# Performance work log

Measured on AMD Instinct MI355X. Metric: run time of the kernel, lower is better.

Reference implementation:

```python
import jax, jax.numpy as jnp
import numpy as np
from functools import partial

B, S, T = 32, 64, 64
VS, VT = 32000, 32000
E, H = 256, 512            # embed_dim, encoder hidden per direction
DH = 2 * H                 # decoder hidden (= encoder_hidden_dim)
A = 128                    # attention_dim


def _p(key, shape, scale=0.05):
    return scale * jax.random.normal(key, shape, dtype=jnp.float32)


def setup_inputs() -> dict:
    key = jax.random.key(0)
    ks = jax.random.split(key, 32)
    inp = {
        'src': jax.random.randint(ks[0], (B, S), 0, VS),
        'tgt_input': jax.random.randint(ks[1], (B, T), 0, VT),
        # encoder
        'enc_emb': _p(ks[2], (VS, E)),
        'enc_Wih_f': _p(ks[3], (4 * H, E)), 'enc_Whh_f': _p(ks[4], (4 * H, H)),
        'enc_bih_f': _p(ks[5], (4 * H,)),  'enc_bhh_f': _p(ks[6], (4 * H,)),
        'enc_Wih_b': _p(ks[7], (4 * H, E)), 'enc_Whh_b': _p(ks[8], (4 * H, H)),
        'enc_bih_b': _p(ks[9], (4 * H,)),  'enc_bhh_b': _p(ks[10], (4 * H,)),
        # decoder
        'dec_emb': _p(ks[11], (VT, E)),
        'Wd': _p(ks[12], (A, DH)), 'bd': _p(ks[13], (A,)),
        'We': _p(ks[14], (A, DH)), 'be': _p(ks[15], (A,)),
        'v_att': _p(ks[16], (A,)), 'bv': _p(ks[17], ()),
        'dec_Wih': _p(ks[18], (4 * DH, E + DH)), 'dec_Whh': _p(ks[19], (4 * DH, DH)),
        'dec_bih': _p(ks[20], (4 * DH,)), 'dec_bhh': _p(ks[21], (4 * DH,)),
        'Wo': _p(ks[22], (VT, DH + DH)), 'bo': _p(ks[23], (VT,)),
    }
    return inp


def _lstm_cell(x, h, c, Wih, Whh, b):
    g = x @ Wih.T + h @ Whh.T + b
    i, f, gg, o = jnp.split(g, 4, axis=-1)  # PyTorch gate order: i,f,g,o
    i, f, o = jax.nn.sigmoid(i), jax.nn.sigmoid(f), jax.nn.sigmoid(o)
    c_new = f * c + i * jnp.tanh(gg)
    h_new = o * jnp.tanh(c_new)
    return h_new, c_new


def _lstm_scan(xs, Wih, Whh, b, reverse):
    # xs: [S,B,E] -> outputs [S,B,H] aligned with input positions, final (h,c)
    h0 = jnp.zeros((xs.shape[1], Whh.shape[1]), xs.dtype)
    def step(carry, x):
        h, c = carry
        h, c = _lstm_cell(x, h, c, Wih, Whh, b)
        return (h, c), h
    (hT, cT), hs = jax.lax.scan(step, (h0, h0), xs, reverse=reverse)
    return hs, hT, cT


def _forward(src, tgt_input, enc_emb,
             enc_Wih_f, enc_Whh_f, enc_bih_f, enc_bhh_f,
             enc_Wih_b, enc_Whh_b, enc_bih_b, enc_bhh_b,
             dec_emb, Wd, bd, We, be, v_att, bv,
             dec_Wih, dec_Whh, dec_bih, dec_bhh, Wo, bo):
    # ---- Encoder: bidirectional single-layer LSTM ----
    emb = enc_emb[src]                              # [B,S,E]
    xs = emb.transpose(1, 0, 2)                     # [S,B,E]
    hs_f, hT_f, cT_f = _lstm_scan(xs, enc_Wih_f, enc_Whh_f, enc_bih_f + enc_bhh_f, False)
    hs_b, hT_b, cT_b = _lstm_scan(xs, enc_Wih_b, enc_Whh_b, enc_bih_b + enc_bhh_b, True)
    enc_out = jnp.concatenate([hs_f, hs_b], axis=-1).transpose(1, 0, 2)  # [B,S,2H]
    h = jnp.concatenate([hT_f, hT_b], axis=-1)      # [B,DH]
    c = jnp.concatenate([cT_f, cT_b], axis=-1)

    # ---- Decoder with Bahdanau attention (full teacher forcing) ----
    enc_proj = enc_out @ We.T + be                  # [B,S,A] precomputed
    dec_b = dec_bih + dec_bhh
    tgt_emb = dec_emb[tgt_input].transpose(1, 0, 2)  # [T,B,E]

    def dec_step(carry, emb_t):
        h, c = carry
        dproj = h @ Wd.T + bd                       # [B,A]
        energy = jnp.tanh(dproj[:, None, :] + enc_proj)  # [B,S,A]
        scores = energy @ v_att + bv                # [B,S]
        w = jax.nn.softmax(scores, axis=1)
        ctx = jnp.einsum('bs,bsh->bh', w, enc_out)  # [B,DH]
        x = jnp.concatenate([emb_t, ctx], axis=-1)  # [B,E+DH]
        h_new, c_new = _lstm_cell(x, h, c, dec_Wih, dec_Whh, dec_b)
        logits = jnp.concatenate([h_new, ctx], axis=-1) @ Wo.T + bo  # [B,VT]
        return (h_new, c_new), logits

    _, logits = jax.lax.scan(dec_step, (h, c), tgt_emb)  # [T,B,VT]
    return logits.transpose(1, 0, 2)                     # [B,T,VT]


def reference(src, tgt_input, enc_emb,
              enc_Wih_f, enc_Whh_f, enc_bih_f, enc_bhh_f,
              enc_Wih_b, enc_Whh_b, enc_bih_b, enc_bhh_b,
              dec_emb, Wd, bd, We, be, v_att, bv,
              dec_Wih, dec_Whh, dec_bih, dec_bhh, Wo, bo):
    return _forward(src, tgt_input, enc_emb,
                    enc_Wih_f, enc_Whh_f, enc_bih_f, enc_bhh_f,
                    enc_Wih_b, enc_Whh_b, enc_bih_b, enc_bhh_b,
                    dec_emb, Wd, bd, We, be, v_att, bv,
                    dec_Wih, dec_Whh, dec_bih, dec_bhh, Wo, bo)
```

## Files before the change

### kernel.cpp

```cpp
#include <hip/hip_runtime.h>


using u16 = unsigned short;
using u32 = unsigned int;
using u64 = unsigned long long;
using f32x4 = __attribute__((ext_vector_type(4))) float;
using s16x8 = __attribute__((ext_vector_type(8))) short;
using u16x4 = __attribute__((ext_vector_type(4))) unsigned short;

__device__ __forceinline__ float sigm_(float x) { return 1.0f / (1.0f + expf(-x)); }
__device__ __forceinline__ float tanh_(float x) {
    float e = __expf(fminf(2.0f * x, 30.0f));
    return (e - 1.0f) / (e + 1.0f);
}

__device__ __forceinline__ u16 f2bf(float x) {
    u32 u = __float_as_uint(x);
    u += 0x7fffu + ((u >> 16) & 1u);
    return (u16)(u >> 16);
}
__device__ __forceinline__ u32 pk2(float a, float b) {
    return (u32)f2bf(a) | ((u32)f2bf(b) << 16);
}
__device__ __forceinline__ float bf2f(u16 v) {
    return __uint_as_float((u32)v << 16);
}

__device__ __forceinline__ void ast32(u32* p, u32 v) {
    __hip_atomic_store(p, v, __ATOMIC_RELAXED, __HIP_MEMORY_SCOPE_AGENT);
}

#define MFMA __builtin_amdgcn_mfma_f32_16x16x32_bf16

#define GLL(g, l) __builtin_amdgcn_global_load_lds( \
    (__attribute__((address_space(1))) void*)(g),   \
    (__attribute__((address_space(3))) void*)(l), 16, 0, 0)

__device__ __forceinline__ void gbar(int* cnt, int target) {
    asm volatile("s_waitcnt vmcnt(0) lgkmcnt(0)" ::: "memory");
    __syncthreads();
    if (threadIdx.x == 0) {
        __hip_atomic_fetch_add(cnt, 1, __ATOMIC_RELAXED, __HIP_MEMORY_SCOPE_AGENT);
        while (__hip_atomic_load(cnt, __ATOMIC_RELAXED, __HIP_MEMORY_SCOPE_AGENT) < target)
            __builtin_amdgcn_s_sleep(1);
    }
    __syncthreads();
}

__global__ __launch_bounds__(256) void k_zero(float* __restrict__ p, int n) {
    int i = blockIdx.x * 256 + threadIdx.x;
    if (i < n) p[i] = 0.0f;
}

__global__ __launch_bounds__(256) void k_cast_bf16(const float* __restrict__ in,
                                                   u16* __restrict__ outp, int n8) {
    int idx = blockIdx.x * 256 + threadIdx.x;
    if (idx >= n8) return;
    const f32x4* p = (const f32x4*)in + (size_t)idx * 2;
    f32x4 a = p[0], c = p[1];
    u32* o = (u32*)(outp + (size_t)idx * 8);
    o[0] = pk2(a.x, a.y); o[1] = pk2(a.z, a.w);
    o[2] = pk2(c.x, c.y); o[3] = pk2(c.z, c.w);
}

__global__ __launch_bounds__(256) void k_embed_bf(const int* __restrict__ tok,
                                                  const float* __restrict__ emb,
                                                  u16* __restrict__ outp) {
    int idx = blockIdx.x * 256 + threadIdx.x;
    int r = idx >> 6, e4 = idx & 63;
    int outer = r >> 5, b = r & 31;
    int tk = tok[b * 64 + outer];
    f32x4 v = ((const f32x4*)emb)[(size_t)tk * 64 + e4];
    u32* o = (u32*)(outp + (size_t)r * 256 + (e4 << 2));
    o[0] = pk2(v.x, v.y); o[1] = pk2(v.z, v.w);
}

__global__ __launch_bounds__(256) void k_prep_perm(
    const float* __restrict__ src, u16* __restrict__ dst,
    int J, int K4, int srcStride, int srcOff, int total)
{
    int idx = blockIdx.x * 256 + threadIdx.x;
    if (idx >= total) return;
    int n = idx / K4, kq = (idx - n * K4) << 2;
    int orig = (n & 3) * J + (n >> 2);
    f32x4 v = *(const f32x4*)(src + (size_t)orig * srcStride + srcOff + kq);
    u32* o = (u32*)(dst + (size_t)n * (K4 << 2) + kq);
    o[0] = pk2(v.x, v.y); o[1] = pk2(v.z, v.w);
}

__global__ __launch_bounds__(256) void k_prep_ws(
    const float* __restrict__ W, u16* __restrict__ dst)
{
    int idx = blockIdx.x * 256 + threadIdx.x;
    int n = idx >> 8, kp = idx & 255, k0 = kp << 1;
    int orig = (n & 3) * 512 + (n >> 2);
    const float* s = W + (size_t)orig * 512 + k0;
    int g = n >> 5, r = n & 31;
    int byteoff = (k0 << 1) ^ ((r & 7) << 4);
    *(u32*)((char*)dst + (size_t)g * 32768 + r * 1024 + byteoff) = pk2(s[0], s[1]);
}

__global__ __launch_bounds__(256) void k_prep_w2s(
    const float* __restrict__ Whh, const float* __restrict__ Wih, u16* __restrict__ dst)
{
    int idx = blockIdx.x * 256 + threadIdx.x;
    int n = idx >> 10, kp = idx & 1023, k0 = kp << 1;
    int orig = (n & 3) * 1024 + (n >> 2);
    const float* s = (k0 < 1024) ? (Whh + (size_t)orig * 1024 + k0)
                                 : (Wih + (size_t)orig * 1280 + 256 + (k0 - 1024));
    int g = n >> 5, r = n & 31;
    int byteoff = (k0 << 1) ^ ((r & 7) << 4);
    *(u32*)((char*)dst + (size_t)g * 131072 + r * 4096 + byteoff) = pk2(s[0], s[1]);
}

__global__ __launch_bounds__(256) void k_gemm_bf(
    const u16* __restrict__ A, const u16* __restrict__ B, int K,
    const float* __restrict__ b1, const float* __restrict__ b2, int biasJ,
    float* __restrict__ C, int ldc, int nM, int nN, int remapOut, int swz)
{
    __shared__ __align__(16) u16 As[128 * 32];
    __shared__ __align__(16) u16 Bs[128 * 32];
    int w = blockIdx.x;
    if (swz) { int cpx = (nM * nN) >> 3; w = (w & 7) * cpx + (w >> 3); }
    int bm = (w % nM) * 128, bn = (w / nM) * 128;
    int tid = threadIdx.x, wave = tid >> 6, lane = tid & 63;
    int wm = wave & 1, wn = wave >> 1;
    f32x4 acc[4][4] = {};

    int rA = wave * 32 + (lane >> 2);
    int cb2 = (lane & 3) * 16;
    const char* gA = (const char*)A + ((size_t)(bm + rA) * K) * 2 + cb2;
    const char* gB = (const char*)B + ((size_t)(bn + rA) * K) * 2 + cb2;
    size_t rowskip = (size_t)16 * K * 2;
    char* lA = (char*)As + wave * 2048;
    char* lB = (char*)Bs + wave * 2048;
    const u16* rdA = As + (wm * 64 + (lane & 15)) * 32 + (lane >> 4) * 8;
    const u16* rdB = Bs + (wn * 64 + (lane & 15)) * 32 + (lane >> 4) * 8;

    for (int k0 = 0; k0 < K; k0 += 32) {
        size_t kb = (size_t)k0 * 2;
        GLL(gA + kb, lA); GLL(gA + kb + rowskip, lA + 1024);
        GLL(gB + kb, lB); GLL(gB + kb + rowskip, lB + 1024);
        __syncthreads();
        s16x8 af[4], bfv[4];
#pragma unroll
        for (int m2 = 0; m2 < 4; ++m2) af[m2] = *(const s16x8*)(rdA + m2 * 512);
#pragma unroll
        for (int n2 = 0; n2 < 4; ++n2) bfv[n2] = *(const s16x8*)(rdB + n2 * 512);
#pragma unroll
        for (int m2 = 0; m2 < 4; ++m2)
#pragma unroll
            for (int n2 = 0; n2 < 4; ++n2)
                acc[m2][n2] = MFMA(af[m2], bfv[n2], acc[m2][n2], 0, 0, 0);
        __syncthreads();
    }

    int rbase = bm + wm * 64 + ((lane >> 4) << 2);
    int cbase = bn + wn * 64 + (lane & 15);
#pragma unroll
    for (int n2 = 0; n2 < 4; ++n2) {
        int col = cbase + n2 * 16;
        int bcol = biasJ ? ((col & 3) * biasJ + (col >> 2)) : col;
        float bias = (b1 ? b1[bcol] : 0.0f) + (b2 ? b2[bcol] : 0.0f);
#pragma unroll
        for (int m2 = 0; m2 < 4; ++m2) {
            f32x4 v = acc[m2][n2];
#pragma unroll
            for (int jj = 0; jj < 4; ++jj) {
                int row = rbase + m2 * 16 + jj;
                int orow = remapOut ? ((row & 31) * 64 + (row >> 5)) : row;
                C[(size_t)orow * ldc + col] = v[jj] + bias;
            }
        }
    }
}

__global__ __launch_bounds__(256, 1) void k_enc_persist(
    const u16* __restrict__ Wsf, const u16* __restrict__ Wsb,
    const float* __restrict__ Gfp, const float* __restrict__ Gbp,
    u16* __restrict__ henc,
    float* __restrict__ cfb,
    u16* __restrict__ encbf,
    int* __restrict__ bar)
{
    __shared__ __align__(16) char smem[50176];
    int tid = threadIdx.x, lane = tid & 63, q = tid >> 6;
    int dir = blockIdx.x >> 6, g = blockIdx.x & 63;
    const char* wsrc = (const char*)(dir ? Wsb : Wsf) + (size_t)g * 32768;
#pragma unroll
    for (int it = 0; it < 8; ++it)
        GLL(wsrc + it * 4096 + tid * 16, smem + it * 4096 + tid * 16);
    __syncthreads();

    float* sacc = (float*)(smem + 32768);
    u16* hst = (u16*)(smem + 49664);
    const float* Gp = dir ? Gbp : Gfp;
    float* cB = cfb + dir * 16384;
    int lr = lane & 15, lk = (lane >> 4) << 3;
    int bb = tid & 31, jl = tid >> 5;
    int n0 = g * 32, j = g * 8 + jl;
    int bi = 0;

    for (int s = 0; s < 64; ++s) {
        const u16* hA = henc + (size_t)s * 32768 + dir * 16384;
        s16x8 afr[8];
#pragma unroll
        for (int it = 0; it < 4; ++it) {
            int ke = q * 128 + it * 32 + lk;
            afr[2 * it]     = *(const s16x8*)(hA + lr * 512 + ke);
            afr[2 * it + 1] = *(const s16x8*)(hA + (lr + 16) * 512 + ke);
        }
        f32x4 acc00 = {}, acc01 = {}, acc10 = {}, acc11 = {};
#pragma unroll
        for (int it = 0; it < 4; ++it) {
            int ke = q * 128 + it * 32 + lk;
            int kb = ke << 1;
            s16x8 b0 = *(const s16x8*)(smem + lr * 1024 + (kb ^ ((lr & 7) << 4)));
            int r1 = lr + 16;
            s16x8 b1 = *(const s16x8*)(smem + r1 * 1024 + (kb ^ ((r1 & 7) << 4)));
            acc00 = MFMA(afr[2 * it], b0, acc00, 0, 0, 0);
            acc01 = MFMA(afr[2 * it], b1, acc01, 0, 0, 0);
            acc10 = MFMA(afr[2 * it + 1], b0, acc10, 0, 0, 0);
            acc11 = MFMA(afr[2 * it + 1], b1, acc11, 0, 0, 0);
        }
        int rw = (lane >> 4) << 2;
#pragma unroll
        for (int rr = 0; rr < 4; ++rr) {
            sacc[q * 1056 + (rw + rr) * 33 + lr]        = acc00[rr];
            sacc[q * 1056 + (rw + rr) * 33 + 16 + lr]   = acc01[rr];
            sacc[q * 1056 + (16 + rw + rr) * 33 + lr]      = acc10[rr];
            sacc[q * 1056 + (16 + rw + rr) * 33 + 16 + lr] = acc11[rr];
        }
        __syncthreads();
        {
            int t = dir ? (63 - s) : s;
            int c4 = jl << 2;
            float gi = 0, gf = 0, gg = 0, go2 = 0;
#pragma unroll
            for (int q2 = 0; q2 < 4; ++q2) {
                const float* sp = sacc + q2 * 1056 + bb * 33 + c4;
                gi += sp[0]; gf += sp[1]; gg += sp[2]; go2 += sp[3];
            }
            f32x4 p4 = *(const f32x4*)(Gp + ((size_t)(t * 32 + bb)) * 2048 + n0 + c4);
            gi += p4.x; gf += p4.y; gg += p4.z; go2 += p4.w;
            float* cp = cB + bb * 512 + j;
            float cn = sigm_(gf) * cp[0] + sigm_(gi) * tanhf(gg);
            cp[0] = cn;
            float h = sigm_(go2) * tanhf(cn);
            u16 h16 = f2bf(h);
            encbf[((size_t)(bb * 64 + t)) * 1024 + dir * 512 + j] = h16;
            hst[bb * 8 + jl] = h16;
        }
        __syncthreads();
        if (tid < 128) {
            int bb2 = tid >> 2, p2 = tid & 3;
            u32 wv = (u32)hst[bb2 * 8 + 2 * p2] | ((u32)hst[bb2 * 8 + 2 * p2 + 1] << 16);
            ast32((u32*)(henc + (size_t)(s + 1) * 32768 + dir * 16384) + bb2 * 256 + g * 4 + p2, wv);
        }
        gbar(bar, (++bi) * 128);
    }
}

__global__ __launch_bounds__(256) void k_dec_init(
    const u16* __restrict__ henc, const float* __restrict__ cfb,
    u16* __restrict__ hcarr, float* __restrict__ cd)
{
    int idx = blockIdx.x * 256 + threadIdx.x;
    int b = idx >> 10, j = idx & 1023;
    int dir = (j >> 9), jj = j & 511;
    hcarr[b * 2048 + j] = henc[(size_t)64 * 32768 + dir * 16384 + b * 512 + jj];
    cd[b * 1024 + j] = cfb[dir * 16384 + b * 512 + jj];
}

__global__ __launch_bounds__(256, 1) void k_dec_persist(
    const u16* __restrict__ W2s, const u16* __restrict__ encbf,
    const float* __restrict__ Prep,
    const u16* __restrict__ Wd_bf, const float* __restrict__ bd,
    const float* __restrict__ eproj, const float* __restrict__ v_att,
    const float* __restrict__ bv,
    u16* __restrict__ hcarr, float* __restrict__ cd, u16* __restrict__ Abf,
    int* __restrict__ bar)
{
    __shared__ __align__(16) char smem[148480];
    int blk = blockIdx.x, tid = threadIdx.x, lane = tid & 63, q = tid >> 6;
    bool isgate = blk < 128;
    {
        const char* src = isgate ? ((const char*)W2s + (size_t)blk * 131072)
                                 : ((const char*)encbf + (size_t)(blk - 128) * 131072);
#pragma unroll
        for (int it = 0; it < 32; ++it)
            GLL(src + it * 4096 + tid * 16, smem + it * 4096 + tid * 16);
    }
    __syncthreads();

    float* sacc = (float*)(smem + 131072);
    u16* hst    = (u16*)(smem + 147968);
    float* hsh  = (float*)(smem + 131072);
    float* red  = (float*)(smem + 135168);
    float* dp   = (float*)(smem + 136192);
    float* sc   = (float*)(smem + 136704);

    int lr = lane & 15, lk = (lane >> 4) << 3;
    int bb = tid & 31, jl = tid >> 5;
    int n0 = blk * 32, j = blk * 8 + jl;
    int b = blk - 128;
    int bi = 0;

    for (int t = 0; t < 64; ++t) {
        const u16* hcT = hcarr + (size_t)t * 65536;
        f32x4 acc00 = {}, acc01 = {}, acc10 = {}, acc11 = {};
        f32x4 p4;
        if (isgate) {
            p4 = *(const f32x4*)(Prep + ((size_t)(t * 32 + bb)) * 4096 + n0 + (jl << 2));
            s16x8 afr[16];
#pragma unroll
            for (int it = 0; it < 8; ++it) {
                int ke = q * 256 + it * 32 + lk;
                afr[2 * it]     = *(const s16x8*)(hcT + lr * 2048 + ke);
                afr[2 * it + 1] = *(const s16x8*)(hcT + (lr + 16) * 2048 + ke);
            }
#pragma unroll
            for (int it = 0; it < 8; ++it) {
                int ke = q * 256 + it * 32 + lk;
                int kb = ke << 1;
                s16x8 b0 = *(const s16x8*)(smem + lr * 4096 + (kb ^ ((lr & 7) << 4)));
                int r1 = lr + 16;
                s16x8 b1 = *(const s16x8*)(smem + r1 * 4096 + (kb ^ ((r1 & 7) << 4)));
                acc00 = MFMA(afr[2 * it], b0, acc00, 0, 0, 0);
                acc01 = MFMA(afr[2 * it], b1, acc01, 0, 0, 0);
                acc10 = MFMA(afr[2 * it + 1], b0, acc10, 0, 0, 0);
                acc11 = MFMA(afr[2 * it + 1], b1, acc11, 0, 0, 0);
            }
        } else {
            {
                u16x4 hv = *(const u16x4*)(hcT + b * 2048 + (tid << 2));
                hsh[(tid << 2) + 0] = bf2f(hv.x);
                hsh[(tid << 2) + 1] = bf2f(hv.y);
                hsh[(tid << 2) + 2] = bf2f(hv.z);
                hsh[(tid << 2) + 3] = bf2f(hv.w);
            }
            __syncthreads();
            {
                int a = tid & 127, half = tid >> 7;
                const u16* wr = Wd_bf + ((size_t)a << 10) + (half << 9);
                const float* hh = hsh + (half << 9);
                float s0 = 0, s1 = 0, s2 = 0, s3 = 0;
#pragma unroll 4
                for (int k = 0; k < 512; k += 32) {
                    s16x8 w0 = *(const s16x8*)(wr + k);
                    s16x8 w1 = *(const s16x8*)(wr + k + 8);
                    s16x8 w2 = *(const s16x8*)(wr + k + 16);
                    s16x8 w3 = *(const s16x8*)(wr + k + 24);
#pragma unroll
                    for (int e = 0; e < 8; ++e) {
                        s0 += bf2f((u16)w0[e]) * hh[k + e];
                        s1 += bf2f((u16)w1[e]) * hh[k + 8 + e];
                        s2 += bf2f((u16)w2[e]) * hh[k + 16 + e];
                        s3 += bf2f((u16)w3[e]) * hh[k + 24 + e];
                    }
                }
                red[tid] = (s0 + s1) + (s2 + s3);
            }
            __syncthreads();
            if (tid < 128) dp[tid] = red[tid] + red[tid + 128] + bd[tid];
            __syncthreads();
            {
                int si = tid >> 2, qq = tid & 3;
                const float* ep = eproj + ((size_t)(b * 64 + si)) * 128 + qq * 32;
                float s = 0.0f;
#pragma unroll 8
                for (int a2 = 0; a2 < 32; ++a2)
                    s += v_att[qq * 32 + a2] * tanh_(dp[qq * 32 + a2] + ep[a2]);
                red[tid] = s;
            }
            __syncthreads();
            if (tid < 64) {
                float x = red[tid * 4] + red[tid * 4 + 1] + red[tid * 4 + 2] + red[tid * 4 + 3] + bv[0];
                float mx = x;
#pragma unroll
                for (int off = 32; off; off >>= 1) mx = fmaxf(mx, __shfl_xor(mx, off));
                float e = __expf(x - mx), ss = e;
#pragma unroll
                for (int off = 32; off; off >>= 1) ss += __shfl_xor(ss, off);
                sc[tid] = e / ss;
            }
            __syncthreads();
            {
                const u16* eL = (const u16*)smem;
                int c0i = tid << 2;
                float c0 = 0, c1 = 0, c2 = 0, c3 = 0;
                for (int s2 = 0; s2 < 64; ++s2) {
                    float wgt = sc[s2];
                    u16x4 rp = *(const u16x4*)(eL + s2 * 1024 + c0i);
                    c0 += wgt * bf2f(rp.x); c1 += wgt * bf2f(rp.y);
                    c2 += wgt * bf2f(rp.z); c3 += wgt * bf2f(rp.w);
                }
                u32 w0 = pk2(c0, c1), w1 = pk2(c2, c3);
                u32* hw = (u32*)hcT + b * 1024 + 512 + (tid << 1);
                ast32(hw, w0); ast32(hw + 1, w1);
                u32* aw = (u32*)(Abf + ((size_t)(t * 32 + b)) * 2048 + 1024 + c0i);
                aw[0] = w0; aw[1] = w1;
            }
        }
        gbar(bar, (++bi) * 160);
        if (isgate) {
            s16x8 afr[16];
#pragma unroll
            for (int it = 0; it < 8; ++it) {
                int ke = 1024 + q * 256 + it * 32 + lk;
                afr[2 * it]     = *(const s16x8*)(hcT + lr * 2048 + ke);
                afr[2 * it + 1] = *(const s16x8*)(hcT + (lr + 16) * 2048 + ke);
            }
#pragma unroll
            for (int it = 0; it < 8; ++it) {
                int ke = 1024 + q * 256 + it * 32 + lk;
                int kb = ke << 1;
                s16x8 b0 = *(const s16x8*)(smem + lr * 4096 + (kb ^ ((lr & 7) << 4)));
                int r1 = lr + 16;
                s16x8 b1 = *(const s16x8*)(smem + r1 * 4096 + (kb ^ ((r1 & 7) << 4)));
                acc00 = MFMA(afr[2 * it], b0, acc00, 0, 0, 0);
                acc01 = MFMA(afr[2 * it], b1, acc01, 0, 0, 0);
                acc10 = MFMA(afr[2 * it + 1], b0, acc10, 0, 0, 0);
                acc11 = MFMA(afr[2 * it + 1], b1, acc11, 0, 0, 0);
            }
            int rw = (lane >> 4) << 2;
#pragma unroll
            for (int rr = 0; rr < 4; ++rr) {
                sacc[q * 1056 + (rw + rr) * 33 + lr]        = acc00[rr];
                sacc[q * 1056 + (rw + rr) * 33 + 16 + lr]   = acc01[rr];
                sacc[q * 1056 + (16 + rw + rr) * 33 + lr]      = acc10[rr];
                sacc[q * 1056 + (16 + rw + rr) * 33 + 16 + lr] = acc11[rr];
            }
            __syncthreads();
            {
                int c4 = jl << 2;
                float gi = 0, gf = 0, gg = 0, go2 = 0;
#pragma unroll
                for (int q2 = 0; q2 < 4; ++q2) {
                    const float* sp = sacc + q2 * 1056 + bb * 33 + c4;
                    gi += sp[0]; gf += sp[1]; gg += sp[2]; go2 += sp[3];
                }
                gi += p4.x; gf += p4.y; gg += p4.z; go2 += p4.w;
                int ci = bb * 1024 + j;
                float cn = sigm_(gf) * cd[ci] + sigm_(gi) * tanhf(gg);
                cd[ci] = cn;
                float h = sigm_(go2) * tanhf(cn);
                u16 h16 = f2bf(h);
                Abf[((size_t)(t * 32 + bb)) * 2048 + j] = h16;
                hst[bb * 8 + jl] = h16;
            }
            __syncthreads();
            if (tid < 128) {
                int bb2 = tid >> 2, p2 = tid & 3;
                u32 wv = (u32)hst[bb2 * 8 + 2 * p2] | ((u32)hst[bb2 * 8 + 2 * p2 + 1] << 16);
                ast32((u32*)(hcarr + (size_t)(t + 1) * 65536) + bb2 * 1024 + blk * 4 + p2, wv);
            }
        }
        gbar(bar, (++bi) * 160);
    }
}

extern "C" void kernel_launch(void* const* d_in, const int* in_sizes, int n_in,
                              void* d_out, int out_size, void* d_ws, size_t ws_size,
                              hipStream_t stream)
{
    (void)in_sizes; (void)n_in; (void)out_size; (void)ws_size;
    const int*   src     = (const int*)d_in[0];
    const int*   tgt     = (const int*)d_in[1];
    const float* enc_emb = (const float*)d_in[2];
    const float* eWih_f  = (const float*)d_in[3];
    const float* eWhh_f  = (const float*)d_in[4];
    const float* ebih_f  = (const float*)d_in[5];
    const float* ebhh_f  = (const float*)d_in[6];
    const float* eWih_b  = (const float*)d_in[7];
    const float* eWhh_b  = (const float*)d_in[8];
    const float* ebih_b  = (const float*)d_in[9];
    const float* ebhh_b  = (const float*)d_in[10];
    const float* dec_emb = (const float*)d_in[11];
    const float* Wd      = (const float*)d_in[12];
    const float* bd      = (const float*)d_in[13];
    const float* We      = (const float*)d_in[14];
    const float* be      = (const float*)d_in[15];
    const float* v_att   = (const float*)d_in[16];
    const float* bv      = (const float*)d_in[17];
    const float* dWih    = (const float*)d_in[18];
    const float* dWhh    = (const float*)d_in[19];
    const float* dbih    = (const float*)d_in[20];
    const float* dbhh    = (const float*)d_in[21];
    const float* Wo      = (const float*)d_in[22];
    const float* bo      = (const float*)d_in[23];
    float* out = (float*)d_out;

    char* wp = (char*)d_ws;
    auto alloc = [&](size_t nbytes) -> void* {
        void* p = (void*)wp;
        wp += (nbytes + 255) & ~(size_t)255;
        return p;
    };
    u16*   Xe_bf = (u16*)alloc(2048u * 256 * 2);
    u16*   Ed_bf = (u16*)alloc(2048u * 256 * 2);
    float* Gf_p  = (float*)alloc(2048u * 2048 * 4);
    float* Gb_p  = (float*)alloc(2048u * 2048 * 4);
    float* Pre_p = (float*)alloc(2048u * 4096 * 4);
    float* zr    = (float*)alloc(131584u);
    float* cfb   = zr;
    int*   cnts  = (int*)((char*)zr + 131072);
    u16*   henc  = (u16*)alloc(65u * 32768 * 2);
    u16*   hcarr = (u16*)alloc(65u * 65536 * 2);
    u16*   encbf = (u16*)alloc(2048u * 1024 * 2);
    float* eproj = (float*)alloc(2048u * 128 * 4);
    float* cd    = (float*)alloc(32768u * 4);
    u16*   Abf   = (u16*)alloc(2048u * 2048 * 2);
    u16*   Wbf   = (u16*)alloc(32000u * 2048 * 2);
    u16*   W2s   = (u16*)alloc(4096u * 2048 * 2);
    u16*   Wsf   = (u16*)alloc(2048u * 512 * 2);
    u16*   Wsb   = (u16*)alloc(2048u * 512 * 2);
    u16*   Wembf = (u16*)alloc(2048u * 256 * 2);
    u16*   Wembb = (u16*)alloc(2048u * 256 * 2);
    u16*   Wembd = (u16*)alloc(4096u * 256 * 2);
    u16*   We_bf = (u16*)alloc(128u * 1024 * 2);
    u16*   Wd_bf = (u16*)alloc(128u * 1024 * 2);

    k_zero<<<129, 256, 0, stream>>>(zr, 32896);
    k_zero<<<64, 256, 0, stream>>>((float*)henc, 16384);

    k_cast_bf16<<<32000, 256, 0, stream>>>(Wo, Wbf, 8192000);
    k_cast_bf16<<<64, 256, 0, stream>>>(We, We_bf, 16384);
    k_cast_bf16<<<64, 256, 0, stream>>>(Wd, Wd_bf, 16384);
    k_prep_perm<<<512, 256, 0, stream>>>(eWih_f, Wembf, 512, 64, 256, 0, 131072);
    k_prep_perm<<<512, 256, 0, stream>>>(eWih_b, Wembb, 512, 64, 256, 0, 131072);
    k_prep_perm<<<1024, 256, 0, stream>>>(dWih, Wembd, 1024, 64, 1280, 0, 262144);
    k_prep_ws<<<2048, 256, 0, stream>>>(eWhh_f, Wsf);
    k_prep_ws<<<2048, 256, 0, stream>>>(eWhh_b, Wsb);
    k_prep_w2s<<<16384, 256, 0, stream>>>(dWhh, dWih, W2s);

    k_embed_bf<<<512, 256, 0, stream>>>(src, enc_emb, Xe_bf);
    k_embed_bf<<<512, 256, 0, stream>>>(tgt, dec_emb, Ed_bf);

    k_gemm_bf<<<256, 256, 0, stream>>>(Xe_bf, Wembf, 256, ebih_f, ebhh_f, 512,
                                       Gf_p, 2048, 16, 16, 0, 1);
    k_gemm_bf<<<256, 256, 0, stream>>>(Xe_bf, Wembb, 256, ebih_b, ebhh_b, 512,
                                       Gb_p, 2048, 16, 16, 0, 1);
    k_gemm_bf<<<512, 256, 0, stream>>>(Ed_bf, Wembd, 256, dbih, dbhh, 1024,
                                       Pre_p, 4096, 16, 32, 0, 1);

    k_enc_persist<<<128, 256, 0, stream>>>(Wsf, Wsb, Gf_p, Gb_p, henc, cfb, encbf, cnts);

    k_gemm_bf<<<16, 256, 0, stream>>>(encbf, We_bf, 1024, be, nullptr, 0,
                                      eproj, 128, 16, 1, 0, 1);
    k_dec_init<<<128, 256, 0, stream>>>(henc, cfb, hcarr, cd);

    k_dec_persist<<<160, 256, 0, stream>>>(W2s, encbf, Pre_p, Wd_bf, bd, eproj,
                                           v_att, bv, hcarr, cd, Abf, cnts + 64);

    k_gemm_bf<<<4000, 256, 0, stream>>>(Abf, Wbf, 2048, bo, nullptr, 0,
                                        out, 32000, 16, 250, 1, 1);
}
```

Measured before the change: 2.375 ms.

## Replace global barriers with per-step producer/consumer flags in persistent LSTM kernels

Swaps the counter-based grid barrier for per-step arrival counters that raise a go flag when the last block arrives. Consumers poll only that flag. In the decoder, gate blocks wait only on the attention blocks' context flag for the current step, and attention blocks wait only on the gate blocks' h flag. This removes one of the two full barriers per step and lets the h-part matmul overlap with the attention computation. The encoder also prefetches the precomputed gate input before the matmul. The cost is more synchronization memory to zero, and correctness now depends on flag ordering under relaxed atomics.

```diff
diff --git a/kernel.cpp b/kernel.cpp
--- a/kernel.cpp
+++ b/kernel.cpp
@@ -36,15 +36,23 @@
     (__attribute__((address_space(1))) void*)(g),   \
     (__attribute__((address_space(3))) void*)(l), 16, 0, 0)
 
-__device__ __forceinline__ void gbar(int* cnt, int target) {
+__device__ __forceinline__ void poll_go(const int* go) {
+    if (threadIdx.x == 0) {
+        while (__hip_atomic_load(go, __ATOMIC_RELAXED, __HIP_MEMORY_SCOPE_AGENT) == 0)
+            __builtin_amdgcn_s_sleep(2);
+    }
+    __syncthreads();
+    asm volatile("" ::: "memory");
+}
+
+__device__ __forceinline__ void arrive_sig(int* cnt, int* go, int n) {
     asm volatile("s_waitcnt vmcnt(0) lgkmcnt(0)" ::: "memory");
     __syncthreads();
     if (threadIdx.x == 0) {
-        __hip_atomic_fetch_add(cnt, 1, __ATOMIC_RELAXED, __HIP_MEMORY_SCOPE_AGENT);
-        while (__hip_atomic_load(cnt, __ATOMIC_RELAXED, __HIP_MEMORY_SCOPE_AGENT) < target)
-            __builtin_amdgcn_s_sleep(1);
-    }
-    __syncthreads();
+        int old = __hip_atomic_fetch_add(cnt, 1, __ATOMIC_RELAXED, __HIP_MEMORY_SCOPE_AGENT);
+        if (old == n - 1)
+            __hip_atomic_store(go, 1, __ATOMIC_RELAXED, __HIP_MEMORY_SCOPE_AGENT);
+    }
 }
 
 __global__ __launch_bounds__(256) void k_zero(float* __restrict__ p, int n) {
@@ -181,7 +189,7 @@
     u16* __restrict__ henc,
     float* __restrict__ cfb,
     u16* __restrict__ encbf,
-    int* __restrict__ bar)
+    int* __restrict__ cntE, int* __restrict__ goE)
 {
     __shared__ __align__(16) char smem[50176];
     int tid = threadIdx.x, lane = tid & 63, q = tid >> 6;
@@ -199,9 +207,11 @@
     int lr = lane & 15, lk = (lane >> 4) << 3;
     int bb = tid & 31, jl = tid >> 5;
     int n0 = g * 32, j = g * 8 + jl;
-    int bi = 0;
 
     for (int s = 0; s < 64; ++s) {
+        if (s) poll_go(goE + s * 16);
+        int t = dir ? (63 - s) : s;
+        f32x4 p4 = *(const f32x4*)(Gp + ((size_t)(t * 32 + bb)) * 2048 + n0 + (jl << 2));
         const u16* hA = henc + (size_t)s * 32768 + dir * 16384;
         s16x8 afr[8];
 #pragma unroll
@@ -233,7 +243,6 @@
         }
         __syncthreads();
         {
-            int t = dir ? (63 - s) : s;
             int c4 = jl << 2;
             float gi = 0, gf = 0, gg = 0, go2 = 0;
 #pragma unroll
@@ -241,7 +250,6 @@
                 const float* sp = sacc + q2 * 1056 + bb * 33 + c4;
                 gi += sp[0]; gf += sp[1]; gg += sp[2]; go2 += sp[3];
             }
-            f32x4 p4 = *(const f32x4*)(Gp + ((size_t)(t * 32 + bb)) * 2048 + n0 + c4);
             gi += p4.x; gf += p4.y; gg += p4.z; go2 += p4.w;
             float* cp = cB + bb * 512 + j;
             float cn = sigm_(gf) * cp[0] + sigm_(gi) * tanhf(gg);
@@ -257,7 +265,7 @@
             u32 wv = (u32)hst[bb2 * 8 + 2 * p2] | ((u32)hst[bb2 * 8 + 2 * p2 + 1] << 16);
             ast32((u32*)(henc + (size_t)(s + 1) * 32768 + dir * 16384) + bb2 * 256 + g * 4 + p2, wv);
         }
-        gbar(bar, (++bi) * 128);
+        arrive_sig(cntE + (s + 1) * 16, goE + (s + 1) * 16, 128);
     }
 }
 
@@ -279,7 +287,8 @@
     const float* __restrict__ eproj, const float* __restrict__ v_att,
     const float* __restrict__ bv,
     u16* __restrict__ hcarr, float* __restrict__ cd, u16* __restrict__ Abf,
-    int* __restrict__ bar)
+    int* __restrict__ hCnt, int* __restrict__ goH,
+    int* __restrict__ ctxCnt, int* __restrict__ goCtx)
 {
     __shared__ __align__(16) char smem[148480];
     int blk = blockIdx.x, tid = threadIdx.x, lane = tid & 63, q = tid >> 6;
@@ -304,14 +313,12 @@
     int bb = tid & 31, jl = tid >> 5;
     int n0 = blk * 32, j = blk * 8 + jl;
     int b = blk - 128;
-    int bi = 0;
 
     for (int t = 0; t < 64; ++t) {
+        if (t) poll_go(goH + t * 16);
         const u16* hcT = hcarr + (size_t)t * 65536;
-        f32x4 acc00 = {}, acc01 = {}, acc10 = {}, acc11 = {};
-        f32x4 p4;
         if (isgate) {
-            p4 = *(const f32x4*)(Prep + ((size_t)(t * 32 + bb)) * 4096 + n0 + (jl << 2));
+            f32x4 p4 = *(const f32x4*)(Prep + ((size_t)(t * 32 + bb)) * 4096 + n0 + (jl << 2));
             s16x8 afr[16];
 #pragma unroll
             for (int it = 0; it < 8; ++it) {
@@ -319,6 +326,7 @@
                 afr[2 * it]     = *(const s16x8*)(hcT + lr * 2048 + ke);
                 afr[2 * it + 1] = *(const s16x8*)(hcT + (lr + 16) * 2048 + ke);
             }
+            f32x4 acc00 = {}, acc01 = {}, acc10 = {}, acc11 = {};
 #pragma unroll
             for (int it = 0; it < 8; ++it) {
                 int ke = q * 256 + it * 32 + lk;
@@ -331,6 +339,58 @@
                 acc10 = MFMA(afr[2 * it + 1], b0, acc10, 0, 0, 0);
                 acc11 = MFMA(afr[2 * it + 1], b1, acc11, 0, 0, 0);
             }
+            poll_go(goCtx + t * 16);
+#pragma unroll
+            for (int it = 0; it < 8; ++it) {
+                int ke = 1024 + q * 256 + it * 32 + lk;
+                afr[2 * it]     = *(const s16x8*)(hcT + lr * 2048 + ke);
+                afr[2 * it + 1] = *(const s16x8*)(hcT + (lr + 16) * 2048 + ke);
+            }
+#pragma unroll
+            for (int it = 0; it < 8; ++it) {
+                int ke = 1024 + q * 256 + it * 32 + lk;
+                int kb = ke << 1;
+                s16x8 b0 = *(const s16x8*)(smem + lr * 4096 + (kb ^ ((lr & 7) << 4)));
+                int r1 = lr + 16;
+                s16x8 b1 = *(const s16x8*)(smem + r1 * 4096 + (kb ^ ((r1 & 7) << 4)));
+                acc00 = MFMA(afr[2 * it], b0, acc00, 0, 0, 0);
+                acc01 = MFMA(afr[2 * it], b1, acc01, 0, 0, 0);
+                acc10 = MFMA(afr[2 * it + 1], b0, acc10, 0, 0, 0);
+                acc11 = MFMA(afr[2 * it + 1], b1, acc11, 0, 0, 0);
+            }
+            int rw = (lane >> 4) << 2;
+#pragma unroll
+            for (int rr = 0; rr < 4; ++rr) {
+                sacc[q * 1056 + (rw + rr) * 33 + lr]        = acc00[rr];
+                sacc[q * 1056 + (rw + rr) * 33 + 16 + lr]   = acc01[rr];
+                sacc[q * 1056 + (16 + rw + rr) * 33 + lr]      = acc10[rr];
+                sacc[q * 1056 + (16 + rw + rr) * 33 + 16 + lr] = acc11[rr];
+            }
+            __syncthreads();
+            {
+                int c4 = jl << 2;
+                float gi = 0, gf = 0, gg = 0, go2 = 0;
+#pragma unroll
+                for (int q2 = 0; q2 < 4; ++q2) {
+                    const float* sp = sacc + q2 * 1056 + bb * 33 + c4;
+                    gi += sp[0]; gf += sp[1]; gg += sp[2]; go2 += sp[3];
+                }
+                gi += p4.x; gf += p4.y; gg += p4.z; go2 += p4.w;
+                int ci = bb * 1024 + j;
+                float cn = sigm_(gf) * cd[ci] + sigm_(gi) * tanhf(gg);
+                cd[ci] = cn;
+                float h = sigm_(go2) * tanhf(cn);
+                u16 h16 = f2bf(h);
+                Abf[((size_t)(t * 32 + bb)) * 2048 + j] = h16;
+                hst[bb * 8 + jl] = h16;
+            }
+            __syncthreads();
+            if (tid < 128) {
+                int bb2 = tid >> 2, p2 = tid & 3;
+                u32 wv = (u32)hst[bb2 * 8 + 2 * p2] | ((u32)hst[bb2 * 8 + 2 * p2 + 1] << 16);
+                ast32((u32*)(hcarr + (size_t)(t + 1) * 65536) + bb2 * 1024 + blk * 4 + p2, wv);
+            }
+            arrive_sig(hCnt + (t + 1) * 16, goH + (t + 1) * 16, 128);
         } else {
             {
                 u16x4 hv = *(const u16x4*)(hcT + b * 2048 + (tid << 2));
@@ -401,62 +461,8 @@
                 u32* aw = (u32*)(Abf + ((size_t)(t * 32 + b)) * 2048 + 1024 + c0i);
                 aw[0] = w0; aw[1] = w1;
             }
-        }
-        gbar(bar, (++bi) * 160);
-        if (isgate) {
-            s16x8 afr[16];
-#pragma unroll
-            for (int it = 0; it < 8; ++it) {
-                int ke = 1024 + q * 256 + it * 32 + lk;
-                afr[2 * it]     = *(const s16x8*)(hcT + lr * 2048 + ke);
-                afr[2 * it + 1] = *(const s16x8*)(hcT + (lr + 16) * 2048 + ke);
-            }
-#pragma unroll
-            for (int it = 0; it < 8; ++it) {
-                int ke = 1024 + q * 256 + it * 32 + lk;
-                int kb = ke << 1;
-                s16x8 b0 = *(const s16x8*)(smem + lr * 4096 + (kb ^ ((lr & 7) << 4)));
-                int r1 = lr + 16;
-                s16x8 b1 = *(const s16x8*)(smem + r1 * 4096 + (kb ^ ((r1 & 7) << 4)));
-                acc00 = MFMA(afr[2 * it], b0, acc00, 0, 0, 0);
-                acc01 = MFMA(afr[2 * it], b1, acc01, 0, 0, 0);
-                acc10 = MFMA(afr[2 * it + 1], b0, acc10, 0, 0, 0);
-                acc11 = MFMA(afr[2 * it + 1], b1, acc11, 0, 0, 0);
-            }
-            int rw = (lane >> 4) << 2;
-#pragma unroll
-            for (int rr = 0; rr < 4; ++rr) {
-                sacc[q * 1056 + (rw + rr) * 33 + lr]        = acc00[rr];
-                sacc[q * 1056 + (rw + rr) * 33 + 16 + lr]   = acc01[rr];
-                sacc[q * 1056 + (16 + rw + rr) * 33 + lr]      = acc10[rr];
-                sacc[q * 1056 + (16 + rw + rr) * 33 + 16 + lr] = acc11[rr];
-            }
-            __syncthreads();
-            {
-                int c4 = jl << 2;
-                float gi = 0, gf = 0, gg = 0, go2 = 0;
-#pragma unroll
-                for (int q2 = 0; q2 < 4; ++q2) {
-                    const float* sp = sacc + q2 * 1056 + bb * 33 + c4;
-                    gi += sp[0]; gf += sp[1]; gg += sp[2]; go2 += sp[3];
-                }
-                gi += p4.x; gf += p4.y; gg += p4.z; go2 += p4.w;
-                int ci = bb * 1024 + j;
-                float cn = sigm_(gf) * cd[ci] + sigm_(gi) * tanhf(gg);
-                cd[ci] = cn;
-                float h = sigm_(go2) * tanhf(cn);
-                u16 h16 = f2bf(h);
-                Abf[((size_t)(t * 32 + bb)) * 2048 + j] = h16;
-                hst[bb * 8 + jl] = h16;
-            }
-            __syncthreads();
-            if (tid < 128) {
-                int bb2 = tid >> 2, p2 = tid & 3;
-                u32 wv = (u32)hst[bb2 * 8 + 2 * p2] | ((u32)hst[bb2 * 8 + 2 * p2 + 1] << 16);
-                ast32((u32*)(hcarr + (size_t)(t + 1) * 65536) + bb2 * 1024 + blk * 4 + p2, wv);
-            }
-        }
-        gbar(bar, (++bi) * 160);
+            arrive_sig(ctxCnt + t * 16, goCtx + t * 16, 32);
+        }
     }
 }
 
@@ -502,9 +508,15 @@
     float* Gf_p  = (float*)alloc(2048u * 2048 * 4);
     float* Gb_p  = (float*)alloc(2048u * 2048 * 4);
     float* Pre_p = (float*)alloc(2048u * 4096 * 4);
-    float* zr    = (float*)alloc(131584u);
+    float* zr    = (float*)alloc(155904u);
     float* cfb   = zr;
-    int*   cnts  = (int*)((char*)zr + 131072);
+    char*  sy    = (char*)zr + 131072;
+    int*   cntE  = (int*)(sy);
+    int*   goE   = (int*)(sy + 4160);
+    int*   hCnt  = (int*)(sy + 8320);
+    int*   goH   = (int*)(sy + 12480);
+    int*   ctxCnt= (int*)(sy + 16640);
+    int*   goCtx = (int*)(sy + 20736);
     u16*   henc  = (u16*)alloc(65u * 32768 * 2);
     u16*   hcarr = (u16*)alloc(65u * 65536 * 2);
     u16*   encbf = (u16*)alloc(2048u * 1024 * 2);
@@ -521,7 +533,7 @@
     u16*   We_bf = (u16*)alloc(128u * 1024 * 2);
     u16*   Wd_bf = (u16*)alloc(128u * 1024 * 2);
 
-    k_zero<<<129, 256, 0, stream>>>(zr, 32896);
+    k_zero<<<153, 256, 0, stream>>>(zr, 38976);
     k_zero<<<64, 256, 0, stream>>>((float*)henc, 16384);
 
     k_cast_bf16<<<32000, 256, 0, stream>>>(Wo, Wbf, 8192000);
@@ -544,14 +556,16 @@
     k_gemm_bf<<<512, 256, 0, stream>>>(Ed_bf, Wembd, 256, dbih, dbhh, 1024,
                                        Pre_p, 4096, 16, 32, 0, 1);
 
-    k_enc_persist<<<128, 256, 0, stream>>>(Wsf, Wsb, Gf_p, Gb_p, henc, cfb, encbf, cnts);
+    k_enc_persist<<<128, 256, 0, stream>>>(Wsf, Wsb, Gf_p, Gb_p, henc, cfb, encbf,
+                                           cntE, goE);
 
     k_gemm_bf<<<16, 256, 0, stream>>>(encbf, We_bf, 1024, be, nullptr, 0,
                                       eproj, 128, 16, 1, 0, 1);
     k_dec_init<<<128, 256, 0, stream>>>(henc, cfb, hcarr, cd);
 
     k_dec_persist<<<160, 256, 0, stream>>>(W2s, encbf, Pre_p, Wd_bf, bd, eproj,
-                                           v_att, bv, hcarr, cd, Abf, cnts + 64);
+                                           v_att, bv, hcarr, cd, Abf,
+                                           hCnt, goH, ctxCnt, goCtx);
 
     k_gemm_bf<<<4000, 256, 0, stream>>>(Abf, Wbf, 2048, bo, nullptr, 0,
                                         out, 32000, 16, 250, 1, 1);
```

Measured after the change: 2.090 ms. 1.14x faster.
